# Kernel tuning notes

Measured on AMD Instinct MI355X. Metric: run time of the kernel, lower is better.

Reference implementation:

```python
import jax, jax.numpy as jnp
import numpy as np

B, C, H, W = 32, 3, 224, 224
P = 14            # n_patches per side
PS = H // P       # 16
D = 768           # embed_size
NH = 12           # heads
DH = D // NH      # 64
L = 12            # n_blocks
FF = 4 * D
OUT = 1000
S = P * P + 1     # 197 tokens


def positional_encoding(seq_len, d):
    i = jnp.arange(seq_len, dtype=jnp.float32)[:, None]
    j = jnp.arange(d, dtype=jnp.float32)[None, :]
    je = jnp.where(j % 2 == 0, j, j - 1)
    ang = i / jnp.power(10000.0, je / d)
    return jnp.where(j % 2 == 0, jnp.sin(ang), jnp.cos(ang))


def layernorm(x, g, b, eps=1e-5):
    mu = jnp.mean(x, axis=-1, keepdims=True)
    var = jnp.var(x, axis=-1, keepdims=True)
    return (x - mu) * jax.lax.rsqrt(var + eps) * g + b


def setup_inputs() -> dict:
    key = jax.random.key(0)
    ks = jax.random.split(key, 20)
    s = 0.02
    inp = {
        'images': jax.random.normal(ks[0], (B, C, H, W), jnp.float32),
        'W_patch': jax.random.normal(ks[1], (D, C * PS * PS), jnp.float32) * s,
        'b_patch': jnp.zeros((D,), jnp.float32),
        'class_token': jax.random.uniform(ks[2], (1, D), jnp.float32),
        'ln1_g': jnp.ones((L, D), jnp.float32),
        'ln1_b': jnp.zeros((L, D), jnp.float32),
        'Wq': jax.random.normal(ks[3], (L, NH, DH, DH), jnp.float32) * s,
        'bq': jnp.zeros((L, NH, DH), jnp.float32),
        'Wk': jax.random.normal(ks[4], (L, NH, DH, DH), jnp.float32) * s,
        'bk': jnp.zeros((L, NH, DH), jnp.float32),
        'Wv': jax.random.normal(ks[5], (L, NH, DH, DH), jnp.float32) * s,
        'bv': jnp.zeros((L, NH, DH), jnp.float32),
        'ln2_g': jnp.ones((L, D), jnp.float32),
        'ln2_b': jnp.zeros((L, D), jnp.float32),
        'W1': jax.random.normal(ks[6], (L, FF, D), jnp.float32) * s,
        'b1': jnp.zeros((L, FF), jnp.float32),
        'W2': jax.random.normal(ks[7], (L, D, FF), jnp.float32) * s,
        'b2': jnp.zeros((L, D), jnp.float32),
        'Wo': jax.random.normal(ks[8], (OUT, D), jnp.float32) * s,
        'bo': jnp.zeros((OUT,), jnp.float32),
    }
    return inp


def reference(images, W_patch, b_patch, class_token, ln1_g, ln1_b,
              Wq, bq, Wk, bk, Wv, bv, ln2_g, ln2_b, W1, b1, W2, b2, Wo, bo):
    b = images.shape[0]
    # patch extraction: [B,C,P,ps,P,ps] -> [B,P*P, C*ps*ps] (flatten order C,h,w)
    patches = images.reshape(b, C, P, PS, P, PS).transpose(0, 2, 4, 1, 3, 5)
    patches = patches.reshape(b, P * P, C * PS * PS)
    tokens = patches @ W_patch.T + b_patch                     # [B, P^2, D]
    cls = jnp.broadcast_to(class_token[None], (b, 1, D))
    x = jnp.concatenate([cls, tokens], axis=1)                 # [B, S, D]
    x = x + positional_encoding(S, D)

    scale = 1.0 / jnp.sqrt(jnp.float32(DH))
    for l in range(L):
        h = layernorm(x, ln1_g[l], ln1_b[l])
        hh = h.reshape(b, S, NH, DH)
        q = jnp.einsum('bshd,hed->bshe', hh, Wq[l]) + bq[l]
        k = jnp.einsum('bshd,hed->bshe', hh, Wk[l]) + bk[l]
        v = jnp.einsum('bshd,hed->bshe', hh, Wv[l]) + bv[l]
        scores = jnp.einsum('bshe,bthe->bhst', q, k) * scale   # [B,H,S,S]
        attn = jax.nn.softmax(scores, axis=-1)
        o = jnp.einsum('bhst,bthe->bshe', attn, v).reshape(b, S, D)
        x = x + o
        h2 = layernorm(x, ln2_g[l], ln2_b[l])
        ff = jax.nn.gelu(h2 @ W1[l].T + b1[l], approximate=False) @ W2[l].T + b2[l]
        x = x + ff

    logits = x[:, 0] @ Wo.T + bo                               # [B, OUT]
    return jax.nn.softmax(logits, axis=-1)
```

## Files before the change

kernel.cpp:

```cpp
#include <hip/hip_runtime.h>
#include <math.h>

static constexpr int kB   = 32;
static constexpr int kC   = 3;
static constexpr int kH   = 224;
static constexpr int kW   = 224;
static constexpr int kP   = 14;
static constexpr int kPS  = 16;
static constexpr int kD   = 768;
static constexpr int kNH  = 12;
static constexpr int kDH  = 64;
static constexpr int kL   = 12;
static constexpr int kFF  = 3072;
static constexpr int kOUT = 1000;
static constexpr int kS   = 197;
static constexpr int kTOK = kB * kS;
static constexpr int kNP  = kP * kP;
static constexpr int kMP  = 6400;
static constexpr int kQKV = 3 * kD;

typedef unsigned short u16;
typedef __attribute__((ext_vector_type(4))) float f32x4;
typedef __attribute__((ext_vector_type(8))) short bf16x8;

__device__ __forceinline__ u16 f2bf(float x) {
    unsigned u = __float_as_uint(x);
    return (u16)((u + 0x7FFFu + ((u >> 16) & 1u)) >> 16);
}
__device__ __forceinline__ float bf2f(u16 x) {
    return __uint_as_float((unsigned)x << 16);
}
__device__ __forceinline__ void cp16_async(void* lds, const void* g) {
    __builtin_amdgcn_global_load_lds((const __attribute__((address_space(1))) unsigned*)g,
                                     (__attribute__((address_space(3))) unsigned*)lds,
                                     16, 0, 0);
}

__global__ void vit_posenc(float* __restrict__ pos) {
    int idx = blockIdx.x * 256 + threadIdx.x;
    if (idx >= kS * kD) return;
    int s = idx / kD, d = idx % kD;
    int je = d & ~1;
    double p = pow(10000.0, (double)je / (double)kD);
    float ang = (float)((double)s / p);
    pos[idx] = (d & 1) ? cosf(ang) : sinf(ang);
}

__global__ void vit_im2col_bf16(const float* __restrict__ img, u16* __restrict__ patches) {
    long idx = (long)blockIdx.x * 256 + threadIdx.x;
    if (idx >= (long)kMP * kD) return;
    int col = (int)(idx % kD);
    long rp = idx / kD;
    if (rp >= (long)kB * kNP) { patches[idx] = 0; return; }
    int p = (int)(rp % kNP), b = (int)(rp / kNP);
    int c = col >> 8;
    int rem = col & 255;
    int i = rem >> 4, j = rem & 15;
    int py = p / kP, px = p % kP;
    patches[idx] = f2bf(img[(((long)b * kC + c) * kH + py * kPS + i) * kW + px * kPS + j]);
}

__global__ void vit_assemble(const float* __restrict__ tokens, const float* __restrict__ cls,
                             const float* __restrict__ pos, float* __restrict__ x) {
    long idx = (long)blockIdx.x * 256 + threadIdx.x;
    if (idx >= (long)kMP * kD) return;
    int d = (int)(idx % kD);
    long bs = idx / kD;
    if (bs >= kTOK) { x[idx] = 0.0f; return; }
    int s = (int)(bs % kS);
    long b = bs / kS;
    float v = (s == 0) ? cls[d] : tokens[((long)b * kNP + (s - 1)) * kD + d];
    x[idx] = v + pos[s * kD + d];
}

__global__ void cast_bf16(const float* __restrict__ in, u16* __restrict__ out, long n4) {
    long i = (long)blockIdx.x * 256 + threadIdx.x;
    if (i >= n4) return;
    float4 v = *(const float4*)(in + i * 4);
    *(ushort4*)(out + i * 4) = make_ushort4(f2bf(v.x), f2bf(v.y), f2bf(v.z), f2bf(v.w));
}

__global__ void zero_u16(u16* __restrict__ p, long n) {
    long i = (long)blockIdx.x * 256 + threadIdx.x;
    if (i < n) p[i] = 0;
}

__global__ void build_whb(const float* __restrict__ Wq, const float* __restrict__ Wk,
                          const float* __restrict__ Wv, const float* __restrict__ bq,
                          const float* __restrict__ bk, const float* __restrict__ bv,
                          u16* __restrict__ Wh, float* __restrict__ bh) {
    int idx = blockIdx.x * 256 + threadIdx.x;
    if (idx >= kNH * 192 * 64) return;
    int d = idx & 63;
    int r = (idx >> 6) % 192;
    int h = idx / (192 * 64);
    int sec = r >> 6, e = r & 63;
    const float* W = (sec == 0) ? Wq : (sec == 1) ? Wk : Wv;
    Wh[idx] = f2bf(W[((h << 6) + e) * 64 + d]);
    if (d == 0) {
        const float* bs = (sec == 0) ? bq : (sec == 1) ? bk : bv;
        bh[h * 192 + r] = bs[(h << 6) + e];
    }
}

__global__ __launch_bounds__(256) void vit_ln(const float* __restrict__ x,
                                              const float* __restrict__ g,
                                              const float* __restrict__ b,
                                              u16* __restrict__ out) {
    long t = blockIdx.x;
    const float* xr = x + t * kD;
    int tid = threadIdx.x;
    float v0 = xr[tid], v1 = xr[tid + 256], v2 = xr[tid + 512];
    float s  = v0 + v1 + v2;
    float sq = v0 * v0 + v1 * v1 + v2 * v2;
    #pragma unroll
    for (int o = 32; o; o >>= 1) { s += __shfl_xor(s, o); sq += __shfl_xor(sq, o); }
    __shared__ float red[8];
    int wid = tid >> 6, lane = tid & 63;
    if (lane == 0) { red[wid] = s; red[4 + wid] = sq; }
    __syncthreads();
    s  = red[0] + red[1] + red[2] + red[3];
    sq = red[4] + red[5] + red[6] + red[7];
    float mu  = s * (1.0f / kD);
    float var = sq * (1.0f / kD) - mu * mu;
    float rs  = rsqrtf(var + 1e-5f);
    u16* orow = out + t * kD;
    orow[tid]       = f2bf((v0 - mu) * rs * g[tid]       + b[tid]);
    orow[tid + 256] = f2bf((v1 - mu) * rs * g[tid + 256] + b[tid + 256]);
    orow[tid + 512] = f2bf((v2 - mu) * rs * g[tid + 512] + b[tid + 512]);
}

template <int EPI>
__global__ __launch_bounds__(256) void mm_bt(const u16* __restrict__ A, int lda,
                                             const u16* __restrict__ B, int ldb,
                                             const float* __restrict__ bias,
                                             const float* X, void* Cout, int ldc, int K) {
    __shared__ __align__(16) u16 As[2][4096];
    __shared__ __align__(16) u16 Bs[2][4096];

    const int gx = gridDim.x, gy = gridDim.y;
    const int nwg = gx * gy;
    const int disp = blockIdx.y * gx + blockIdx.x;
    const int q8 = nwg >> 3, r8 = nwg & 7;
    const int xcd = disp & 7, lot = disp >> 3;
    const int work = (xcd < r8 ? xcd * (q8 + 1) : r8 * (q8 + 1) + (xcd - r8) * q8) + lot;
    const int row0 = (work / gy) << 7;
    const int col0 = (work % gy) << 7;

    const int tid  = threadIdx.x;
    const int lane = tid & 63;
    const int wm = ((tid >> 6) >> 1) << 6;
    const int wn = ((tid >> 6) & 1) << 6;
    const int lr = lane & 15, lhi = lane >> 4;

    const int srow = tid >> 2;
    const int sch  = (((tid & 3) ^ ((srow >> 1) & 3)) << 3);
    const u16* Ag = A + (long)(row0 + srow) * lda + sch;
    const u16* Bg = B + (long)(col0 + srow) * ldb + sch;
    const long Astep = 64L * lda, Bstep = 64L * ldb;
    const int ldst = tid << 3;

    f32x4 acc[4][4] = {};
    const int nk = K >> 5;

    cp16_async(&As[0][ldst],        Ag);
    cp16_async(&As[0][ldst + 2048], Ag + Astep);
    cp16_async(&Bs[0][ldst],        Bg);
    cp16_async(&Bs[0][ldst + 2048], Bg + Bstep);
    __syncthreads();

    const int rch = (lhi ^ ((lr >> 1) & 3)) << 3;
    for (int t = 0; t < nk; t++) {
        const int cur = t & 1;
        if (t + 1 < nk) {
            const int k0 = (t + 1) << 5;
            cp16_async(&As[cur ^ 1][ldst],        Ag + k0);
            cp16_async(&As[cur ^ 1][ldst + 2048], Ag + Astep + k0);
            cp16_async(&Bs[cur ^ 1][ldst],        Bg + k0);
            cp16_async(&Bs[cur ^ 1][ldst + 2048], Bg + Bstep + k0);
        }
        bf16x8 af[4], bfr[4];
        #pragma unroll
        for (int m = 0; m < 4; m++)
            af[m] = *(const bf16x8*)&As[cur][(wm + (m << 4) + lr) * 32 + rch];
        #pragma unroll
        for (int n = 0; n < 4; n++)
            bfr[n] = *(const bf16x8*)&Bs[cur][(wn + (n << 4) + lr) * 32 + rch];
        #pragma unroll
        for (int m = 0; m < 4; m++)
            #pragma unroll
            for (int n = 0; n < 4; n++)
                acc[m][n] = __builtin_amdgcn_mfma_f32_16x16x32_bf16(af[m], bfr[n], acc[m][n], 0, 0, 0);
        __syncthreads();
    }

    const int r0 = wm + (lhi << 2);
    const int cb = wn + lr;
    #pragma unroll
    for (int n = 0; n < 4; n++) {
        const int cc = col0 + cb + (n << 4);
        const float bv = bias[cc];
        #pragma unroll
        for (int m = 0; m < 4; m++) {
            #pragma unroll
            for (int r = 0; r < 4; r++) {
                const long idx = (long)(row0 + r0 + (m << 4) + r) * ldc + cc;
                float v = acc[m][n][r] + bv;
                if (EPI == 1) {
                    v = 0.5f * v * (1.0f + erff(v * 0.70710678118654752f));
                    ((u16*)Cout)[idx] = f2bf(v);
                } else if (EPI == 2) {
                    ((float*)Cout)[idx] = v + X[idx];
                } else if (EPI == 3) {
                    ((u16*)Cout)[idx] = f2bf(v);
                } else {
                    ((float*)Cout)[idx] = v;
                }
            }
        }
    }
}

__global__ __launch_bounds__(256) void mm_qkv(const u16* __restrict__ hbm,
                                              const u16* __restrict__ Wh,
                                              const float* __restrict__ bh,
                                              u16* __restrict__ qkv) {
    const int h = blockIdx.y;
    const int row0 = blockIdx.x << 6;
    const int tid = threadIdx.x, lane = tid & 63, wave = tid >> 6;
    const int l15 = lane & 15, lhi = lane >> 4;
    const u16* Ab = hbm + h * kDH + (lhi << 3);
    const u16* Bb = Wh + (long)h * 192 * 64 + (lhi << 3);

    bf16x8 af[4][2];
    #pragma unroll
    for (int m = 0; m < 4; m++) {
        const u16* ap = Ab + (long)(row0 + (m << 4) + l15) * kD;
        af[m][0] = *(const bf16x8*)ap;
        af[m][1] = *(const bf16x8*)(ap + 32);
    }
    bf16x8 bfr[3][2];
    #pragma unroll
    for (int n = 0; n < 3; n++) {
        const u16* bp = Bb + (long)(wave * 48 + (n << 4) + l15) * 64;
        bfr[n][0] = *(const bf16x8*)bp;
        bfr[n][1] = *(const bf16x8*)(bp + 32);
    }
    f32x4 acc[4][3] = {};
    #pragma unroll
    for (int m = 0; m < 4; m++)
        #pragma unroll
        for (int n = 0; n < 3; n++) {
            acc[m][n] = __builtin_amdgcn_mfma_f32_16x16x32_bf16(af[m][0], bfr[n][0], acc[m][n], 0, 0, 0);
            acc[m][n] = __builtin_amdgcn_mfma_f32_16x16x32_bf16(af[m][1], bfr[n][1], acc[m][n], 0, 0, 0);
        }
    #pragma unroll
    for (int n = 0; n < 3; n++) {
        const int c = wave * 48 + (n << 4) + l15;
        const int sec = c >> 6, e = c & 63;
        const float bv = bh[h * 192 + c];
        const long gcol = (long)sec * kD + h * kDH + e;
        #pragma unroll
        for (int m = 0; m < 4; m++)
            #pragma unroll
            for (int i = 0; i < 4; i++) {
                const int r = row0 + (m << 4) + (lhi << 2) + i;
                qkv[(long)r * kQKV + gcol] = f2bf(acc[m][n][i] + bv);
            }
    }
}

__global__ __launch_bounds__(256) void vit_attn_fused(const u16* __restrict__ qkv,
                                                      float* __restrict__ x) {
    constexpr int SP = 224;
    constexpr int NT = 13;
    constexpr int LDP = 232;
    __shared__ u16 Plds[64][LDP];
    __shared__ u16 Vt[64][LDP];

    const int z = blockIdx.y, qt = blockIdx.x;
    const int b = z / kNH, h = z % kNH;
    const u16* base = qkv + (long)b * kS * kQKV;
    const u16* Qg = base + h * kDH;
    const u16* Kg = base + kD + h * kDH;
    const u16* Vg = base + 2 * kD + h * kDH;
    const int tid = threadIdx.x, lane = tid & 63, wave = tid >> 6;
    const int l15 = lane & 15, lhi = lane >> 4;

    for (int i = tid; i < (SP * kDH) / 4; i += 256) {
        int s  = i >> 4;
        int d0 = (i & 15) << 2;
        ushort4 v = *(const ushort4*)(Vg + (long)s * kQKV + d0);
        Vt[d0 + 0][s] = v.x; Vt[d0 + 1][s] = v.y;
        Vt[d0 + 2][s] = v.z; Vt[d0 + 3][s] = v.w;
    }

    const int qrow = (qt << 6) + (wave << 4) + l15;
    const u16* qrp = Qg + (long)qrow * kQKV + (lhi << 3);
    const bf16x8 qf0 = *(const bf16x8*)(qrp);
    const bf16x8 qf1 = *(const bf16x8*)(qrp + 32);

    f32x4 sc[NT];
    const u16* krp = Kg + (long)l15 * kQKV + (lhi << 3);
    #pragma unroll
    for (int t = 0; t < NT; t++) {
        const u16* kp = krp + (long)(t << 4) * kQKV;
        bf16x8 kb0 = *(const bf16x8*)(kp);
        bf16x8 kb1 = *(const bf16x8*)(kp + 32);
        f32x4 a = {0.0f, 0.0f, 0.0f, 0.0f};
        a = __builtin_amdgcn_mfma_f32_16x16x32_bf16(qf0, kb0, a, 0, 0, 0);
        a = __builtin_amdgcn_mfma_f32_16x16x32_bf16(qf1, kb1, a, 0, 0, 0);
        sc[t] = a;
    }

    float mx[4] = {-1e30f, -1e30f, -1e30f, -1e30f};
    #pragma unroll
    for (int t = 0; t < NT; t++) {
        const int c = (t << 4) + l15;
        #pragma unroll
        for (int q = 0; q < 4; q++) {
            float v = (c < kS) ? sc[t][q] * 0.125f : -1e30f;
            sc[t][q] = v;
            mx[q] = fmaxf(mx[q], v);
        }
    }
    #pragma unroll
    for (int o = 1; o < 16; o <<= 1)
        #pragma unroll
        for (int q = 0; q < 4; q++) mx[q] = fmaxf(mx[q], __shfl_xor(mx[q], o));
    float sum[4] = {0.0f, 0.0f, 0.0f, 0.0f};
    #pragma unroll
    for (int t = 0; t < NT; t++)
        #pragma unroll
        for (int q = 0; q < 4; q++) {
            float e = __expf(sc[t][q] - mx[q]);
            sc[t][q] = e;
            sum[q] += e;
        }
    #pragma unroll
    for (int o = 1; o < 16; o <<= 1)
        #pragma unroll
        for (int q = 0; q < 4; q++) sum[q] += __shfl_xor(sum[q], o);

    const int prow = (wave << 4) + (lhi << 2);
    #pragma unroll
    for (int t = 0; t < NT; t++)
        #pragma unroll
        for (int q = 0; q < 4; q++)
            Plds[prow + q][(t << 4) + l15] = f2bf(sc[t][q]);
    #pragma unroll
    for (int q = 0; q < 4; q++)
        Plds[prow + q][208 + l15] = 0;
    __syncthreads();

    f32x4 oacc[4] = {};
    const int arow = (wave << 4) + l15;
    const int koff = lhi << 3;
    #pragma unroll
    for (int ks = 0; ks < 7; ks++) {
        bf16x8 pa = *(const bf16x8*)&Plds[arow][ks * 32 + koff];
        #pragma unroll
        for (int n = 0; n < 4; n++) {
            bf16x8 vb = *(const bf16x8*)&Vt[(n << 4) + l15][ks * 32 + koff];
            oacc[n] = __builtin_amdgcn_mfma_f32_16x16x32_bf16(pa, vb, oacc[n], 0, 0, 0);
        }
    }

    const int orow0 = (qt << 6) + (wave << 4) + (lhi << 2);
    #pragma unroll
    for (int q = 0; q < 4; q++) {
        const int r = orow0 + q;
        if (r >= kS) continue;
        const float rinv = 1.0f / sum[q];
        float* xp = x + ((long)b * kS + r) * kD + h * kDH + l15;
        #pragma unroll
        for (int n = 0; n < 4; n++)
            xp[n << 4] += oacc[n][q] * rinv;
    }
}

template <int ACT, int RES>
__global__ __launch_bounds__(256) void vit_gemm(const float* __restrict__ A, long lda, long sAz,
                                                const float* __restrict__ B, long ldb, long sBz,
                                                const float* __restrict__ bias, long sbz,
                                                const float* __restrict__ R,
                                                float* __restrict__ C, long ldc, long sCz,
                                                int M, int N, int K) {
    __shared__ __align__(16) float As[16][64];
    __shared__ __align__(16) float Bs[16][64];
    long z = blockIdx.z;
    A += z * sAz;  B += z * sBz;  C += z * sCz;
    if (bias) bias += z * sbz;
    const float* Rp = nullptr;
    if (RES) Rp = R + z * sCz;

    int row0 = blockIdx.x * 64, col0 = blockIdx.y * 64;
    int tid = threadIdx.x;
    int lr = tid >> 2, lk = (tid & 3) << 2;
    int tm = tid >> 4, tn = tid & 15;
    float acc[4][4] = {};

    for (int k0 = 0; k0 < K; k0 += 16) {
        float4 a = {0, 0, 0, 0}, bb = {0, 0, 0, 0};
        int gr = row0 + lr;
        if (gr < M) a = *(const float4*)(A + (long)gr * lda + k0 + lk);
        int gc = col0 + lr;
        if (gc < N) bb = *(const float4*)(B + (long)gc * ldb + k0 + lk);
        __syncthreads();
        As[lk + 0][lr] = a.x;  As[lk + 1][lr] = a.y;  As[lk + 2][lr] = a.z;  As[lk + 3][lr] = a.w;
        Bs[lk + 0][lr] = bb.x; Bs[lk + 1][lr] = bb.y; Bs[lk + 2][lr] = bb.z; Bs[lk + 3][lr] = bb.w;
        __syncthreads();
        #pragma unroll
        for (int k = 0; k < 16; k++) {
            const float4 av = *reinterpret_cast<const float4*>(&As[k][tm << 2]);
            const float4 bv = *reinterpret_cast<const float4*>(&Bs[k][tn << 2]);
            float aa[4] = {av.x, av.y, av.z, av.w};
            float bw[4] = {bv.x, bv.y, bv.z, bv.w};
            #pragma unroll
            for (int i = 0; i < 4; i++)
                #pragma unroll
                for (int j = 0; j < 4; j++)
                    acc[i][j] = fmaf(aa[i], bw[j], acc[i][j]);
        }
    }
    #pragma unroll
    for (int i = 0; i < 4; i++) {
        int r = row0 + (tm << 2) + i;
        if (r >= M) continue;
        #pragma unroll
        for (int j = 0; j < 4; j++) {
            int c = col0 + (tn << 2) + j;
            if (c >= N) continue;
            float v = acc[i][j];
            if (bias) v += bias[c];
            if (ACT == 1) v = 0.5f * v * (1.0f + erff(v * 0.70710678118654752f));
            if (RES) v += Rp[(long)r * ldc + c];
            C[(long)r * ldc + c] = v;
        }
    }
}

__global__ __launch_bounds__(256) void vit_smout(const float* __restrict__ logits,
                                                 float* __restrict__ out) {
    int b = blockIdx.x;
    const float* p = logits + (long)b * kOUT;
    int tid = threadIdx.x;
    float v[4];
    float mx = -1e30f;
    #pragma unroll
    for (int i = 0; i < 4; i++) {
        int c = tid + (i << 8);
        v[i] = (c < kOUT) ? p[c] : -1e30f;
        mx = fmaxf(mx, v[i]);
    }
    #pragma unroll
    for (int o = 32; o; o >>= 1) mx = fmaxf(mx, __shfl_xor(mx, o));
    __shared__ float red[8];
    int wid = tid >> 6, lane = tid & 63;
    if (lane == 0) red[wid] = mx;
    __syncthreads();
    mx = fmaxf(fmaxf(red[0], red[1]), fmaxf(red[2], red[3]));
    float sum = 0.0f;
    #pragma unroll
    for (int i = 0; i < 4; i++) {
        int c = tid + (i << 8);
        if (c < kOUT) { v[i] = expf(v[i] - mx); sum += v[i]; }
    }
    #pragma unroll
    for (int o = 32; o; o >>= 1) sum += __shfl_xor(sum, o);
    __syncthreads();
    if (lane == 0) red[4 + wid] = sum;
    __syncthreads();
    sum = red[4] + red[5] + red[6] + red[7];
    float inv = 1.0f / sum;
    #pragma unroll
    for (int i = 0; i < 4; i++) {
        int c = tid + (i << 8);
        if (c < kOUT) out[(long)b * kOUT + c] = v[i] * inv;
    }
}

extern "C" void kernel_launch(void* const* d_in, const int* in_sizes, int n_in,
                              void* d_out, int out_size, void* d_ws, size_t ws_size,
                              hipStream_t stream) {
    (void)in_sizes; (void)n_in; (void)out_size; (void)ws_size;
    const float* images  = (const float*)d_in[0];
    const float* W_patch = (const float*)d_in[1];
    const float* b_patch = (const float*)d_in[2];
    const float* cls     = (const float*)d_in[3];
    const float* ln1_g   = (const float*)d_in[4];
    const float* ln1_b   = (const float*)d_in[5];
    const float* Wq      = (const float*)d_in[6];
    const float* bq      = (const float*)d_in[7];
    const float* Wk      = (const float*)d_in[8];
    const float* bk      = (const float*)d_in[9];
    const float* Wv      = (const float*)d_in[10];
    const float* bv      = (const float*)d_in[11];
    const float* ln2_g   = (const float*)d_in[12];
    const float* ln2_b   = (const float*)d_in[13];
    const float* W1      = (const float*)d_in[14];
    const float* b1      = (const float*)d_in[15];
    const float* W2      = (const float*)d_in[16];
    const float* b2      = (const float*)d_in[17];
    const float* Wo      = (const float*)d_in[18];
    const float* bo      = (const float*)d_in[19];

    char* wsB = (char*)d_ws;
    auto alloc = [&](size_t bytes) { char* p = wsB; wsB += (bytes + 255) & ~(size_t)255; return p; };
    float* pos    = (float*)alloc((size_t)kS * kD * 4);
    float* x      = (float*)alloc((size_t)kMP * kD * 4);
    u16*   hb     = (u16*)  alloc((size_t)kMP * kD * 2);
    u16*   qkvb   = (u16*)  alloc((size_t)kMP * kQKV * 2);
    u16*   ff1b   = (u16*)  alloc((size_t)kMP * kFF * 2);
    u16*   W1b    = (u16*)  alloc((size_t)kFF * kD * 2);
    u16*   W2b    = (u16*)  alloc((size_t)kFF * kD * 2);
    u16*   Whb    = (u16*)  alloc((size_t)kNH * 192 * 64 * 2);
    u16*   Wpb    = (u16*)  alloc((size_t)kD * kD * 2);
    float* bhb    = (float*)alloc((size_t)kNH * 192 * 4);
    float* logits = (float*)alloc((size_t)kB * kOUT * 4);
    float* tokens   = (float*)qkvb;
    u16*   patchesb = ff1b;

    vit_posenc<<<(kS * kD + 255) / 256, 256, 0, stream>>>(pos);
    vit_im2col_bf16<<<(int)(((long)kMP * kD) / 256), 256, 0, stream>>>(images, patchesb);
    cast_bf16<<<(kD * kD / 4 + 255) / 256, 256, 0, stream>>>(W_patch, Wpb, (long)kD * kD / 4);
    zero_u16<<<(96 * kD + 255) / 256, 256, 0, stream>>>(hb + (long)kTOK * kD, 96L * kD);
    mm_bt<0><<<dim3(kMP / 128, kD / 128), 256, 0, stream>>>(
        patchesb, kD, Wpb, kD, b_patch, nullptr, tokens, kD, kD);
    vit_assemble<<<(int)(((long)kMP * kD) / 256), 256, 0, stream>>>(tokens, cls, pos, x);

    for (int l = 0; l < kL; l++) {
        cast_bf16<<<(kFF * kD / 4 + 255) / 256, 256, 0, stream>>>(
            W1 + (long)l * kFF * kD, W1b, (long)kFF * kD / 4);
        cast_bf16<<<(kFF * kD / 4 + 255) / 256, 256, 0, stream>>>(
            W2 + (long)l * kFF * kD, W2b, (long)kFF * kD / 4);
        build_whb<<<(kNH * 192 * 64 + 255) / 256, 256, 0, stream>>>(
            Wq + (long)l * kNH * kDH * kDH, Wk + (long)l * kNH * kDH * kDH,
            Wv + (long)l * kNH * kDH * kDH, bq + (long)l * kNH * kDH,
            bk + (long)l * kNH * kDH, bv + (long)l * kNH * kDH, Whb, bhb);

        vit_ln<<<kTOK, 256, 0, stream>>>(x, ln1_g + (long)l * kD, ln1_b + (long)l * kD, hb);
        mm_qkv<<<dim3(kMP / 64, kNH), 256, 0, stream>>>(hb, Whb, bhb, qkvb);

        vit_attn_fused<<<dim3(4, kB * kNH), 256, 0, stream>>>(qkvb, x);

        vit_ln<<<kTOK, 256, 0, stream>>>(x, ln2_g + (long)l * kD, ln2_b + (long)l * kD, hb);
        mm_bt<1><<<dim3(kMP / 128, kFF / 128), 256, 0, stream>>>(
            hb, kD, W1b, kD, b1 + (long)l * kFF, nullptr, ff1b, kFF, kD);
        mm_bt<2><<<dim3(kMP / 128, kD / 128), 256, 0, stream>>>(
            ff1b, kFF, W2b, kFF, b2 + (long)l * kD, x, x, kD, kFF);
    }

    vit_gemm<0, 0><<<dim3(1, 16, 1), 256, 0, stream>>>(
        x, (long)kS * kD, 0, Wo, kD, 0, bo, 0, nullptr,
        logits, kOUT, 0, kB, kOUT, kD);
    vit_smout<<<kB, 256, 0, stream>>>(logits, (float*)d_out);
}
```

Baseline: 2.770 ms.

## Triple-buffer GEMM LDS pipeline with explicit vmcnt waits and MFMA priority hints

The bf16 GEMM kernel moves from double to triple buffering in LDS. Each tile load is issued two iterations ahead, and explicit s_waitcnt vmcnt counts plus raw s_barrier replace __syncthreads, so global loads stay in flight across the MFMA work. s_setprio hints are also wrapped around the MFMA sections in the QKV and attention kernels to favour matrix-issuing waves. The cost is extra LDS per block, which may lower occupancy, and correctness now depends on the hand-set vmcnt counts.

```diff
diff --git a/kernel.cpp b/kernel.cpp
--- a/kernel.cpp
+++ b/kernel.cpp
@@ -135,8 +135,8 @@
                                              const u16* __restrict__ B, int ldb,
                                              const float* __restrict__ bias,
                                              const float* X, void* Cout, int ldc, int K) {
-    __shared__ __align__(16) u16 As[2][4096];
-    __shared__ __align__(16) u16 Bs[2][4096];
+    __shared__ __align__(16) u16 As[3][4096];
+    __shared__ __align__(16) u16 Bs[3][4096];
 
     const int gx = gridDim.x, gy = gridDim.y;
     const int nwg = gx * gy;
@@ -163,22 +163,22 @@
     f32x4 acc[4][4] = {};
     const int nk = K >> 5;
 
-    cp16_async(&As[0][ldst],        Ag);
-    cp16_async(&As[0][ldst + 2048], Ag + Astep);
-    cp16_async(&Bs[0][ldst],        Bg);
-    cp16_async(&Bs[0][ldst + 2048], Bg + Bstep);
-    __syncthreads();
+    auto stage = [&](int buf, int k0) {
+        cp16_async(&As[buf][ldst],        Ag + k0);
+        cp16_async(&As[buf][ldst + 2048], Ag + Astep + k0);
+        cp16_async(&Bs[buf][ldst],        Bg + k0);
+        cp16_async(&Bs[buf][ldst + 2048], Bg + Bstep + k0);
+    };
+    stage(0, 0);
+    stage(1, 32);
 
     const int rch = (lhi ^ ((lr >> 1) & 3)) << 3;
+    int cur = 0;
     for (int t = 0; t < nk; t++) {
-        const int cur = t & 1;
-        if (t + 1 < nk) {
-            const int k0 = (t + 1) << 5;
-            cp16_async(&As[cur ^ 1][ldst],        Ag + k0);
-            cp16_async(&As[cur ^ 1][ldst + 2048], Ag + Astep + k0);
-            cp16_async(&Bs[cur ^ 1][ldst],        Bg + k0);
-            cp16_async(&Bs[cur ^ 1][ldst + 2048], Bg + Bstep + k0);
-        }
+        if (t + 1 < nk) asm volatile("s_waitcnt vmcnt(4)" ::: "memory");
+        else            asm volatile("s_waitcnt vmcnt(0)" ::: "memory");
+        __builtin_amdgcn_sched_barrier(0);
+        __builtin_amdgcn_s_barrier();
         bf16x8 af[4], bfr[4];
         #pragma unroll
         for (int m = 0; m < 4; m++)
@@ -186,12 +186,17 @@
         #pragma unroll
         for (int n = 0; n < 4; n++)
             bfr[n] = *(const bf16x8*)&Bs[cur][(wn + (n << 4) + lr) * 32 + rch];
+        if (t + 2 < nk) {
+            int nb = cur + 2; if (nb >= 3) nb -= 3;
+            stage(nb, (t + 2) << 5);
+        }
         #pragma unroll
         for (int m = 0; m < 4; m++)
             #pragma unroll
             for (int n = 0; n < 4; n++)
                 acc[m][n] = __builtin_amdgcn_mfma_f32_16x16x32_bf16(af[m], bfr[n], acc[m][n], 0, 0, 0);
-        __syncthreads();
+        __builtin_amdgcn_s_barrier();
+        cur = (cur + 1 == 3) ? 0 : cur + 1;
     }
 
     const int r0 = wm + (lhi << 2);
@@ -247,6 +252,7 @@
         bfr[n][1] = *(const bf16x8*)(bp + 32);
     }
     f32x4 acc[4][3] = {};
+    __builtin_amdgcn_s_setprio(1);
     #pragma unroll
     for (int m = 0; m < 4; m++)
         #pragma unroll
@@ -254,6 +260,7 @@
             acc[m][n] = __builtin_amdgcn_mfma_f32_16x16x32_bf16(af[m][0], bfr[n][0], acc[m][n], 0, 0, 0);
             acc[m][n] = __builtin_amdgcn_mfma_f32_16x16x32_bf16(af[m][1], bfr[n][1], acc[m][n], 0, 0, 0);
         }
+    __builtin_amdgcn_s_setprio(0);
     #pragma unroll
     for (int n = 0; n < 3; n++) {
         const int c = wave * 48 + (n << 4) + l15;
@@ -302,6 +309,7 @@
 
     f32x4 sc[NT];
     const u16* krp = Kg + (long)l15 * kQKV + (lhi << 3);
+    __builtin_amdgcn_s_setprio(1);
     #pragma unroll
     for (int t = 0; t < NT; t++) {
         const u16* kp = krp + (long)(t << 4) * kQKV;
@@ -312,6 +320,7 @@
         a = __builtin_amdgcn_mfma_f32_16x16x32_bf16(qf1, kb1, a, 0, 0, 0);
         sc[t] = a;
     }
+    __builtin_amdgcn_s_setprio(0);
 
     float mx[4] = {-1e30f, -1e30f, -1e30f, -1e30f};
     #pragma unroll
@@ -356,6 +365,7 @@
     f32x4 oacc[4] = {};
     const int arow = (wave << 4) + l15;
     const int koff = lhi << 3;
+    __builtin_amdgcn_s_setprio(1);
     #pragma unroll
     for (int ks = 0; ks < 7; ks++) {
         bf16x8 pa = *(const bf16x8*)&Plds[arow][ks * 32 + koff];
@@ -365,6 +375,7 @@
             oacc[n] = __builtin_amdgcn_mfma_f32_16x16x32_bf16(pa, vb, oacc[n], 0, 0, 0);
         }
     }
+    __builtin_amdgcn_s_setprio(0);
 
     const int orow0 = (qt << 6) + (wave << 4) + (lhi << 2);
     #pragma unroll
```

After: 2.544 ms. 1.09x faster.
